# Performance work log

Measured on AMD Instinct MI355X. Metric: run time of the kernel, lower is better.

The kernel has to match this reference:

```python
import jax, jax.numpy as jnp
import numpy as np

N = 100000
E = 1600000
F_IN = 128
H = 128
NUM_GRAPHS = 512
EPS = 1e-5


def setup_inputs() -> dict:
    key = jax.random.key(0)
    ks = jax.random.split(key, 16)
    x = jax.random.normal(ks[0], (N, F_IN), dtype=jnp.float32)
    edge_index = jax.random.randint(ks[1], (2, E), 0, N, dtype=jnp.int32)
    batch = jnp.sort(jax.random.randint(ks[2], (N,), 0, NUM_GRAPHS, dtype=jnp.int32))
    def lin(k, fi, fo):
        s = 1.0 / np.sqrt(fi)
        return jax.random.uniform(k, (fi, fo), jnp.float32, -s, s)
    return {
        "x": x, "edge_index": edge_index, "batch": batch,
        "W1": lin(ks[3], F_IN, H), "b1": jnp.zeros((H,), jnp.float32),
        "g1": jnp.ones((H,), jnp.float32), "beta1": jnp.zeros((H,), jnp.float32),
        "W2": lin(ks[4], H, H), "b2": jnp.zeros((H,), jnp.float32),
        "g2": jnp.ones((H,), jnp.float32), "beta2": jnp.zeros((H,), jnp.float32),
        "W3": lin(ks[5], H, H), "b3": jnp.zeros((H,), jnp.float32),
        "g3": jnp.ones((H,), jnp.float32), "beta3": jnp.zeros((H,), jnp.float32),
        "Wl": lin(ks[6], H, 1), "bl": jnp.zeros((1,), jnp.float32),
    }


def _layer_norm(x, g, b):
    mu = jnp.mean(x, axis=-1, keepdims=True)
    var = jnp.mean((x - mu) ** 2, axis=-1, keepdims=True)
    return (x - mu) * jax.lax.rsqrt(var + EPS) * g + b


def _gcn_conv(x, W, b, src, dst, dinv):
    # GCNConv: D^{-1/2}(A+I)D^{-1/2} X W + b, deg includes self-loops
    h = x @ W                                   # [N,H]
    enorm = dinv[src] * dinv[dst]               # [E]
    agg = jax.ops.segment_sum(h[src] * enorm[:, None], dst, num_segments=N)
    agg = agg + h * (dinv * dinv)[:, None]      # self-loop contribution
    return agg + b


def reference(x, edge_index, batch, W1, b1, g1, beta1, W2, b2, g2, beta2,
              W3, b3, g3, beta3, Wl, bl):
    src, dst = edge_index[0], edge_index[1]
    deg = 1.0 + jax.ops.segment_sum(jnp.ones((E,), jnp.float32), dst, num_segments=N)
    dinv = jax.lax.rsqrt(deg)
    h = jax.nn.relu(_layer_norm(_gcn_conv(x, W1, b1, src, dst, dinv), g1, beta1))
    h = jax.nn.relu(_layer_norm(_gcn_conv(h, W2, b2, src, dst, dinv), g2, beta2))
    h = jax.nn.relu(_layer_norm(_gcn_conv(h, W3, b3, src, dst, dinv), g3, beta3))
    # global mean pool over graphs
    sums = jax.ops.segment_sum(h, batch, num_segments=NUM_GRAPHS)
    cnts = jax.ops.segment_sum(jnp.ones((N,), jnp.float32), batch, num_segments=NUM_GRAPHS)
    pooled = sums / jnp.maximum(cnts, 1.0)[:, None]
    return pooled @ Wl + bl                     # [NUM_GRAPHS, 1]
```

## Files before the change

kernel.cpp:

```cpp
#include <hip/hip_runtime.h>
#include <hip/hip_bf16.h>
#include <math.h>

#define N_NODES    100000
#define N_EDGES    1600000
#define FDIM       128
#define NUM_GRAPHS 512
#define EPS        1e-5f
#define PADN       100096

#define B_CVT   12512
#define B_WPK   192

#define NBUCK   196
#define CAPA    10240
#define EB_CHUNK 8192
#define BINA_BLOCKS ((N_EDGES + EB_CHUNK - 1) / EB_CHUNK)

typedef __attribute__((ext_vector_type(8))) __bf16 bf16x8;
typedef __attribute__((ext_vector_type(4))) float  f32x4;

__device__ __forceinline__ unsigned short f2bf(float f) {
    unsigned u = __builtin_bit_cast(unsigned, f);
    u += 0x7FFF + ((u >> 16) & 1);
    return (unsigned short)(u >> 16);
}
__device__ __forceinline__ float bf2f(unsigned short b) {
    unsigned u = ((unsigned)b) << 16;
    return __builtin_bit_cast(float, u);
}

__device__ __forceinline__ void dec4(unsigned dw, float* o) {
    auto lo = __builtin_amdgcn_cvt_pk_f32_fp8(dw, false);
    auto hi = __builtin_amdgcn_cvt_pk_f32_fp8(dw, true);
    o[0] = lo[0]; o[1] = lo[1]; o[2] = hi[0]; o[3] = hi[1];
}

__device__ __forceinline__ void acc16(uint4 v, float* a) {
    float d[16];
    dec4(v.x, &d[0]); dec4(v.y, &d[4]); dec4(v.z, &d[8]); dec4(v.w, &d[12]);
#pragma unroll
    for (int f = 0; f < 16; f++) a[f] += d[f];
}


__global__ __launch_bounds__(256) void k_build(const int* __restrict__ src,
                                               const int* __restrict__ dst,
                                               int* __restrict__ bcur,
                                               unsigned* __restrict__ binned,
                                               const float* __restrict__ x,
                                               unsigned short* __restrict__ xb,
                                               const float* __restrict__ W1,
                                               const float* __restrict__ W2,
                                               const float* __restrict__ W3,
                                               unsigned short* __restrict__ wp) {
    int b = blockIdx.x;
    int t = threadIdx.x;
    if (b < BINA_BLOCKS) {
        __shared__ int hist[NBUCK];
        __shared__ int lbase[NBUCK];
        __shared__ int loff[NBUCK];
        int e0 = b * EB_CHUNK;

        for (int j = t; j < NBUCK; j += 256) { hist[j] = 0; loff[j] = 0; }
        __syncthreads();

        for (int k = t; k < EB_CHUNK; k += 256) {
            int e = e0 + k;
            if (e < N_EDGES) atomicAdd(&hist[dst[e] >> 9], 1);
        }
        __syncthreads();
        for (int j = t; j < NBUCK; j += 256)
            lbase[j] = atomicAdd(&bcur[j], hist[j]);
        __syncthreads();

        for (int k = t; k < EB_CHUNK; k += 256) {
            int e = e0 + k;
            if (e < N_EDGES) {
                int d = dst[e];
                int bk = d >> 9;
                int p = lbase[bk] + atomicAdd(&loff[bk], 1);
                binned[(size_t)bk * CAPA + p] = (unsigned)src[e] | ((unsigned)(d & 511) << 17);
            }
        }
    } else if (b < BINA_BLOCKS + B_CVT) {
        long long idx = ((long long)(b - BINA_BLOCKS) * 256 + t) * 4;
        ushort4 o;
        if (idx < (long long)N_NODES * FDIM) {
            float4 v = *(const float4*)(x + idx);
            o.x = f2bf(v.x); o.y = f2bf(v.y); o.z = f2bf(v.z); o.w = f2bf(v.w);
        } else {
            o.x = o.y = o.z = o.w = 0;
        }
        *(ushort4*)(xb + idx) = o;
    } else {
        int wb  = b - (BINA_BLOCKS + B_CVT);
        int mat = wb >> 6;
        const float* W = (mat == 0) ? W1 : (mat == 1) ? W2 : W3;
        unsigned short* o = wp + (size_t)mat * 16384;
        int idx = (wb & 63) * 256 + t;
        int j  = idx & 7;
        int l  = (idx >> 3) & 63;
        int ct = (idx >> 9) & 7;
        int ks = idx >> 12;
        int k  = ks * 32 + (l >> 4) * 8 + j;
        int c  = ct * 16 + (l & 15);
        o[idx] = f2bf(W[k * 128 + c]);
    }
}


__global__ __launch_bounds__(256) void k_bscan(const int* __restrict__ bcur,
                                               int* __restrict__ bbase,
                                               int* __restrict__ offs) {
    __shared__ int lds[256];
    int t = threadIdx.x;
    int v = (t < NBUCK) ? bcur[t] : 0;
    lds[t] = v;
    __syncthreads();
    for (int off = 1; off < 256; off <<= 1) {
        int y = 0;
        if (t >= off) y = lds[t - off];
        __syncthreads();
        if (t >= off) lds[t] += y;
        __syncthreads();
    }
    if (t < NBUCK) bbase[t] = lds[t] - v;
    if (t == 0) offs[N_NODES] = N_EDGES;
}


__global__ __launch_bounds__(256) void k_binB(const unsigned* __restrict__ binned,
                                              const int* __restrict__ bcur,
                                              const int* __restrict__ bbase,
                                              int* __restrict__ offs,
                                              float* __restrict__ dinv,
                                              int* __restrict__ csr_src) {
    __shared__ int cnt_l[512];
    __shared__ int lofs[512];
    __shared__ int part[256];
    __shared__ int stage[CAPA];
    int b = blockIdx.x;
    int t = threadIdx.x;
    int nb0 = b * 512;
    int cnt = bcur[b];
    int seg0 = bbase[b];

    cnt_l[t] = 0; cnt_l[t + 256] = 0;
    __syncthreads();

    for (int k = t; k < cnt; k += 256)
        atomicAdd(&cnt_l[binned[(size_t)b * CAPA + k] >> 17], 1);
    __syncthreads();

    int c0 = cnt_l[2 * t], c1 = cnt_l[2 * t + 1];
    int ps = c0 + c1;
    part[t] = ps;
    __syncthreads();
    for (int off = 1; off < 256; off <<= 1) {
        int y = 0;
        if (t >= off) y = part[t - off];
        __syncthreads();
        if (t >= off) part[t] += y;
        __syncthreads();
    }
    int excl = part[t] - ps;
    lofs[2 * t]     = excl;
    lofs[2 * t + 1] = excl + c0;
    __syncthreads();

    for (int j = t; j < 512; j += 256) {
        int node = nb0 + j;
        if (node < N_NODES) {
            offs[node] = seg0 + lofs[j];
            dinv[node] = rsqrtf(1.0f + (float)cnt_l[j]);
        }
    }
    __syncthreads();

    for (int k = t; k < cnt; k += 256) {
        unsigned v = binned[(size_t)b * CAPA + k];
        int ld = v >> 17;
        int p  = atomicAdd(&lofs[ld], 1);
        stage[p] = (int)(v & 0x1FFFF);
    }
    __syncthreads();
    for (int k = t; k < cnt; k += 256) csr_src[seg0 + k] = stage[k];
}


__global__ __launch_bounds__(256) void k_gemm(const unsigned short* __restrict__ A,
                                              const unsigned short* __restrict__ Wp,
                                              const float* __restrict__ dinv,
                                              unsigned char* __restrict__ C8) {
    int t    = threadIdx.x;
    int lane = t & 63;
    int w    = t >> 6;
    int wc   = w & 1;
    int wr   = w >> 1;
    int rb   = blockIdx.x * 128 + wr * 64 + (lane & 15);
    int koff = (lane >> 4) * 8;

    f32x4 acc[4][4];
#pragma unroll
    for (int c = 0; c < 4; c++)
#pragma unroll
        for (int r = 0; r < 4; r++) acc[c][r] = (f32x4){0.f, 0.f, 0.f, 0.f};

    const bf16x8* Wv = (const bf16x8*)Wp;
#pragma unroll
    for (int ks = 0; ks < 4; ++ks) {
        bf16x8 fw[4], fa[4];
#pragma unroll
        for (int c = 0; c < 4; ++c)
            fw[c] = Wv[(ks * 8 + wc * 4 + c) * 64 + lane];
#pragma unroll
        for (int r = 0; r < 4; ++r) {
            const uint4 v = *(const uint4*)(A + (size_t)(rb + r * 16) * 128 + ks * 32 + koff);
            fa[r] = __builtin_bit_cast(bf16x8, v);
        }
#pragma unroll
        for (int c = 0; c < 4; ++c)
#pragma unroll
            for (int r = 0; r < 4; ++r)
                acc[c][r] = __builtin_amdgcn_mfma_f32_16x16x32_bf16(fw[c], fa[r], acc[c][r], 0, 0, 0);
    }

#pragma unroll
    for (int r = 0; r < 4; ++r) {
        int row = blockIdx.x * 128 + wr * 64 + r * 16 + (lane & 15);
        if (row < N_NODES) {
            float dv = dinv[row];
#pragma unroll
            for (int c = 0; c < 4; ++c) {
                int col = (wc * 4 + c) * 16 + (lane >> 4) * 4;
                unsigned u = __builtin_amdgcn_cvt_pk_fp8_f32(acc[c][r][0] * dv, acc[c][r][1] * dv, 0, false);
                u = (unsigned)__builtin_amdgcn_cvt_pk_fp8_f32(acc[c][r][2] * dv, acc[c][r][3] * dv, (int)u, true);
                *(unsigned*)(C8 + (size_t)row * 128 + col) = u;
            }
        }
    }
}


__global__ __launch_bounds__(256) void k_agg(const unsigned char* __restrict__ h8,
                                             unsigned short* __restrict__ out,
                                             const int* __restrict__ offs,
                                             const int* __restrict__ csr_src,
                                             const float* __restrict__ dinv,
                                             const float* __restrict__ bias,
                                             const float* __restrict__ gamma,
                                             const float* __restrict__ beta) {
    int t    = threadIdx.x;
    int lane = t & 63;
    int grp  = lane >> 3;
    int sl   = lane & 7;
    int i    = blockIdx.x * 32 + (t >> 6) * 8 + grp;

    float di = dinv[i];
    size_t lofs16 = (size_t)sl * 16;

    float a[16];
    {
        uint4 v = *(const uint4*)(h8 + (size_t)i * 128 + lofs16);
        float d[16];
        dec4(v.x, &d[0]); dec4(v.y, &d[4]); dec4(v.z, &d[8]); dec4(v.w, &d[12]);
#pragma unroll
        for (int f = 0; f < 16; f++) a[f] = d[f];
    }

    int e0 = offs[i], e1 = offs[i + 1];
    int e = e0;
    for (; e + 4 <= e1; e += 4) {
        int s0 = csr_src[e + 0];
        int s1 = csr_src[e + 1];
        int s2 = csr_src[e + 2];
        int s3 = csr_src[e + 3];
        uint4 v0 = *(const uint4*)(h8 + (size_t)s0 * 128 + lofs16);
        uint4 v1 = *(const uint4*)(h8 + (size_t)s1 * 128 + lofs16);
        uint4 v2 = *(const uint4*)(h8 + (size_t)s2 * 128 + lofs16);
        uint4 v3 = *(const uint4*)(h8 + (size_t)s3 * 128 + lofs16);
        acc16(v0, a); acc16(v1, a); acc16(v2, a); acc16(v3, a);
    }
    for (; e < e1; ++e) {
        int s = csr_src[e];
        uint4 v = *(const uint4*)(h8 + (size_t)s * 128 + lofs16);
        acc16(v, a);
    }

    float4 b0 = *(const float4*)(bias + sl * 16);
    float4 b1 = *(const float4*)(bias + sl * 16 + 4);
    float4 b2 = *(const float4*)(bias + sl * 16 + 8);
    float4 b3 = *(const float4*)(bias + sl * 16 + 12);
    a[0]  = fmaf(a[0],  di, b0.x); a[1]  = fmaf(a[1],  di, b0.y);
    a[2]  = fmaf(a[2],  di, b0.z); a[3]  = fmaf(a[3],  di, b0.w);
    a[4]  = fmaf(a[4],  di, b1.x); a[5]  = fmaf(a[5],  di, b1.y);
    a[6]  = fmaf(a[6],  di, b1.z); a[7]  = fmaf(a[7],  di, b1.w);
    a[8]  = fmaf(a[8],  di, b2.x); a[9]  = fmaf(a[9],  di, b2.y);
    a[10] = fmaf(a[10], di, b2.z); a[11] = fmaf(a[11], di, b2.w);
    a[12] = fmaf(a[12], di, b3.x); a[13] = fmaf(a[13], di, b3.y);
    a[14] = fmaf(a[14], di, b3.z); a[15] = fmaf(a[15], di, b3.w);

    float s1 = 0.f, s2 = 0.f;
#pragma unroll
    for (int f = 0; f < 16; f++) { s1 += a[f]; s2 += a[f] * a[f]; }
#pragma unroll
    for (int off = 1; off < 8; off <<= 1) {
        s1 += __shfl_xor(s1, off);
        s2 += __shfl_xor(s2, off);
    }
    float mu   = s1 * (1.0f / 128.0f);
    float var  = s2 * (1.0f / 128.0f) - mu * mu;
    float rstd = rsqrtf(var + EPS);

    float g[16], be[16];
    {
        float4 g0 = *(const float4*)(gamma + sl * 16);
        float4 g1 = *(const float4*)(gamma + sl * 16 + 4);
        float4 g2 = *(const float4*)(gamma + sl * 16 + 8);
        float4 g3 = *(const float4*)(gamma + sl * 16 + 12);
        g[0]=g0.x; g[1]=g0.y; g[2]=g0.z; g[3]=g0.w;
        g[4]=g1.x; g[5]=g1.y; g[6]=g1.z; g[7]=g1.w;
        g[8]=g2.x; g[9]=g2.y; g[10]=g2.z; g[11]=g2.w;
        g[12]=g3.x; g[13]=g3.y; g[14]=g3.z; g[15]=g3.w;
        float4 e0v = *(const float4*)(beta + sl * 16);
        float4 e1v = *(const float4*)(beta + sl * 16 + 4);
        float4 e2v = *(const float4*)(beta + sl * 16 + 8);
        float4 e3v = *(const float4*)(beta + sl * 16 + 12);
        be[0]=e0v.x; be[1]=e0v.y; be[2]=e0v.z; be[3]=e0v.w;
        be[4]=e1v.x; be[5]=e1v.y; be[6]=e1v.z; be[7]=e1v.w;
        be[8]=e2v.x; be[9]=e2v.y; be[10]=e2v.z; be[11]=e2v.w;
        be[12]=e3v.x; be[13]=e3v.y; be[14]=e3v.z; be[15]=e3v.w;
    }

    unsigned ow[8];
#pragma unroll
    for (int f = 0; f < 8; f++) {
        float r0 = fmaxf((a[2*f]   - mu) * rstd * g[2*f]   + be[2*f],   0.f);
        float r1 = fmaxf((a[2*f+1] - mu) * rstd * g[2*f+1] + be[2*f+1], 0.f);
        ow[f] = (unsigned)f2bf(r0) | ((unsigned)f2bf(r1) << 16);
    }
    uint4* op = (uint4*)(out + (size_t)i * 128 + sl * 16);
    op[0] = make_uint4(ow[0], ow[1], ow[2], ow[3]);
    op[1] = make_uint4(ow[4], ow[5], ow[6], ow[7]);
}


__global__ __launch_bounds__(256) void k_pool(const unsigned short* __restrict__ h,
                                              const int* __restrict__ batch,
                                              const float* __restrict__ Wl,
                                              const float* __restrict__ bl,
                                              float* __restrict__ out) {
    __shared__ float2 part[4][64];
    int g = blockIdx.x;
    int t = threadIdx.x, w = t >> 6, lane = t & 63;

    int lo = 0, hi = N_NODES;
    while (lo < hi) { int mid = (lo + hi) >> 1; if (batch[mid] < g) lo = mid + 1; else hi = mid; }
    int s = lo;
    lo = s; hi = N_NODES;
    while (lo < hi) { int mid = (lo + hi) >> 1; if (batch[mid] < g + 1) lo = mid + 1; else hi = mid; }
    int e = lo;

    float ax = 0.f, ay = 0.f;
    for (int n = s + w; n < e; n += 4) {
        unsigned v = *(const unsigned*)(h + (size_t)n * 128 + lane * 2);
        ax += bf2f((unsigned short)(v & 0xffff));
        ay += bf2f((unsigned short)(v >> 16));
    }
    part[w][lane] = make_float2(ax, ay);
    __syncthreads();
    if (t < 64) {
        float sx = part[0][lane].x + part[1][lane].x + part[2][lane].x + part[3][lane].x;
        float sy = part[0][lane].y + part[1][lane].y + part[2][lane].y + part[3][lane].y;
        float cnt = fmaxf((float)(e - s), 1.0f);
        float inv = 1.0f / cnt;
        float p = sx * inv * Wl[lane * 2] + sy * inv * Wl[lane * 2 + 1];
#pragma unroll
        for (int off = 32; off; off >>= 1) p += __shfl_xor(p, off);
        if (lane == 0) out[g] = p + bl[0];
    }
}


extern "C" void kernel_launch(void* const* d_in, const int* in_sizes, int n_in,
                              void* d_out, int out_size, void* d_ws, size_t ws_size,
                              hipStream_t stream) {
    const float* x     = (const float*)d_in[0];
    const int*   ei    = (const int*)d_in[1];
    const int*   batch = (const int*)d_in[2];
    const float* W1 = (const float*)d_in[3];
    const float* b1 = (const float*)d_in[4];
    const float* g1 = (const float*)d_in[5];
    const float* be1 = (const float*)d_in[6];
    const float* W2 = (const float*)d_in[7];
    const float* b2 = (const float*)d_in[8];
    const float* g2 = (const float*)d_in[9];
    const float* be2 = (const float*)d_in[10];
    const float* W3 = (const float*)d_in[11];
    const float* b3 = (const float*)d_in[12];
    const float* g3 = (const float*)d_in[13];
    const float* be3 = (const float*)d_in[14];
    const float* Wl = (const float*)d_in[15];
    const float* bl = (const float*)d_in[16];

    const int* src = ei;
    const int* dst = ei + N_EDGES;

    char* ws = (char*)d_ws;
    size_t off = 0;
    auto alloc = [&](size_t bytes) -> void* {
        void* p = ws + off;
        off += (bytes + 255) & ~(size_t)255;
        return p;
    };
    unsigned short* xb   = (unsigned short*)alloc((size_t)PADN * FDIM * 2);
    unsigned short* hA   = (unsigned short*)alloc((size_t)PADN * FDIM * 2);
    unsigned char*  hF   = (unsigned char*)alloc((size_t)PADN * FDIM);
    unsigned short* wp   = (unsigned short*)alloc((size_t)3 * 16384 * 2);
    float* dinv    = (float*)alloc((size_t)N_NODES * 4);
    int*   offs    = (int*)alloc((size_t)(N_NODES + 1) * 4);
    int*   csr_src = (int*)alloc((size_t)N_EDGES * 4);
    unsigned* binned = (unsigned*)alloc((size_t)NBUCK * CAPA * 4);
    int*   bcur    = (int*)alloc(256 * 4);
    int*   bbase   = (int*)alloc(256 * 4);

    hipMemsetAsync(bcur, 0, 256 * 4, stream);

    k_build<<<BINA_BLOCKS + B_CVT + B_WPK, 256, 0, stream>>>(src, dst, bcur, binned,
                                                             x, xb, W1, W2, W3, wp);
    k_bscan<<<1, 256, 0, stream>>>(bcur, bbase, offs);
    k_binB<<<NBUCK, 256, 0, stream>>>(binned, bcur, bbase, offs, dinv, csr_src);

    int gemm_grid = PADN / 128;
    int agg_grid  = N_NODES / 32;

    k_gemm<<<gemm_grid, 256, 0, stream>>>(xb, wp, dinv, hF);
    k_agg<<<agg_grid, 256, 0, stream>>>(hF, hA, offs, csr_src, dinv, b1, g1, be1);
    k_gemm<<<gemm_grid, 256, 0, stream>>>(hA, wp + 16384, dinv, hF);
    k_agg<<<agg_grid, 256, 0, stream>>>(hF, hA, offs, csr_src, dinv, b2, g2, be2);
    k_gemm<<<gemm_grid, 256, 0, stream>>>(hA, wp + 32768, dinv, hF);
    k_agg<<<agg_grid, 256, 0, stream>>>(hF, hA, offs, csr_src, dinv, b3, g3, be3);

    k_pool<<<NUM_GRAPHS, 256, 0, stream>>>(hA, batch, Wl, bl, (float*)d_out);
}
```

Measured before the change: 276.0 us.

## Stage edges in LDS during binning, fold bucket scan into binB, unroll aggregation

The edge binning pass now reads src/dst once, keeps the packed values and bucket ids in shared memory, and reuses them for the scatter step. It also uses smaller chunks so more blocks run in parallel. The separate single-block bucket scan kernel is removed, and each binB block instead computes its own segment base with a wave-reduced prefix over bcur. The aggregation gather loop gains an 8-way unrolled stage so more loads are in flight. The trade-off is smaller chunks, which mean more global atomics on bcur and a less contiguous scatter order, plus extra shared memory and registers.

```diff
diff --git a/kernel.cpp b/kernel.cpp
--- a/kernel.cpp
+++ b/kernel.cpp
@@ -14,7 +14,7 @@
 
 #define NBUCK   196
 #define CAPA    10240
-#define EB_CHUNK 8192
+#define EB_CHUNK 2048
 #define BINA_BLOCKS ((N_EDGES + EB_CHUNK - 1) / EB_CHUNK)
 
 typedef __attribute__((ext_vector_type(8))) __bf16 bf16x8;
@@ -60,28 +60,31 @@
         __shared__ int hist[NBUCK];
         __shared__ int lbase[NBUCK];
         __shared__ int loff[NBUCK];
+        __shared__ unsigned lpack[EB_CHUNK];
+        __shared__ unsigned short lbuck[EB_CHUNK];
         int e0 = b * EB_CHUNK;
+        int nE = min(EB_CHUNK, N_EDGES - e0);
 
         for (int j = t; j < NBUCK; j += 256) { hist[j] = 0; loff[j] = 0; }
         __syncthreads();
 
-        for (int k = t; k < EB_CHUNK; k += 256) {
-            int e = e0 + k;
-            if (e < N_EDGES) atomicAdd(&hist[dst[e] >> 9], 1);
+        for (int k = t; k < nE; k += 256) {
+            int e  = e0 + k;
+            int d  = dst[e];
+            int bk = d >> 9;
+            lpack[k] = (unsigned)src[e] | ((unsigned)(d & 511) << 17);
+            lbuck[k] = (unsigned short)bk;
+            atomicAdd(&hist[bk], 1);
         }
         __syncthreads();
         for (int j = t; j < NBUCK; j += 256)
             lbase[j] = atomicAdd(&bcur[j], hist[j]);
         __syncthreads();
 
-        for (int k = t; k < EB_CHUNK; k += 256) {
-            int e = e0 + k;
-            if (e < N_EDGES) {
-                int d = dst[e];
-                int bk = d >> 9;
-                int p = lbase[bk] + atomicAdd(&loff[bk], 1);
-                binned[(size_t)bk * CAPA + p] = (unsigned)src[e] | ((unsigned)(d & 511) << 17);
-            }
+        for (int k = t; k < nE; k += 256) {
+            int bk = lbuck[k];
+            int p  = lbase[bk] + atomicAdd(&loff[bk], 1);
+            binned[(size_t)bk * CAPA + p] = lpack[k];
         }
     } else if (b < BINA_BLOCKS + B_CVT) {
         long long idx = ((long long)(b - BINA_BLOCKS) * 256 + t) * 4;
@@ -110,29 +113,8 @@
 }
 
 
-__global__ __launch_bounds__(256) void k_bscan(const int* __restrict__ bcur,
-                                               int* __restrict__ bbase,
-                                               int* __restrict__ offs) {
-    __shared__ int lds[256];
-    int t = threadIdx.x;
-    int v = (t < NBUCK) ? bcur[t] : 0;
-    lds[t] = v;
-    __syncthreads();
-    for (int off = 1; off < 256; off <<= 1) {
-        int y = 0;
-        if (t >= off) y = lds[t - off];
-        __syncthreads();
-        if (t >= off) lds[t] += y;
-        __syncthreads();
-    }
-    if (t < NBUCK) bbase[t] = lds[t] - v;
-    if (t == 0) offs[N_NODES] = N_EDGES;
-}
-
-
 __global__ __launch_bounds__(256) void k_binB(const unsigned* __restrict__ binned,
                                               const int* __restrict__ bcur,
-                                              const int* __restrict__ bbase,
                                               int* __restrict__ offs,
                                               float* __restrict__ dinv,
                                               int* __restrict__ csr_src) {
@@ -144,7 +126,19 @@
     int t = threadIdx.x;
     int nb0 = b * 512;
     int cnt = bcur[b];
-    int seg0 = bbase[b];
+
+    int pv = (t < b) ? bcur[t] : 0;
+#pragma unroll
+    for (int off = 32; off; off >>= 1) pv += __shfl_down(pv, off);
+    part[t >> 6] = pv;
+    __syncthreads();
+    int seg0 = part[0];
+    if (t == 0) {
+    }
+    __syncthreads();
+    if ((t & 63) == 0) part[t >> 6] = pv;
+    __syncthreads();
+    seg0 = part[0] + part[1] + part[2] + part[3];
 
     cnt_l[t] = 0; cnt_l[t + 256] = 0;
     __syncthreads();
@@ -176,6 +170,7 @@
             dinv[node] = rsqrtf(1.0f + (float)cnt_l[j]);
         }
     }
+    if (b == NBUCK - 1 && t == 0) offs[N_NODES] = N_EDGES;
     __syncthreads();
 
     for (int k = t; k < cnt; k += 256) {
@@ -271,6 +266,26 @@
 
     int e0 = offs[i], e1 = offs[i + 1];
     int e = e0;
+    for (; e + 8 <= e1; e += 8) {
+        int s0 = csr_src[e + 0];
+        int s1 = csr_src[e + 1];
+        int s2 = csr_src[e + 2];
+        int s3 = csr_src[e + 3];
+        int s4 = csr_src[e + 4];
+        int s5 = csr_src[e + 5];
+        int s6 = csr_src[e + 6];
+        int s7 = csr_src[e + 7];
+        uint4 v0 = *(const uint4*)(h8 + (size_t)s0 * 128 + lofs16);
+        uint4 v1 = *(const uint4*)(h8 + (size_t)s1 * 128 + lofs16);
+        uint4 v2 = *(const uint4*)(h8 + (size_t)s2 * 128 + lofs16);
+        uint4 v3 = *(const uint4*)(h8 + (size_t)s3 * 128 + lofs16);
+        uint4 v4 = *(const uint4*)(h8 + (size_t)s4 * 128 + lofs16);
+        uint4 v5 = *(const uint4*)(h8 + (size_t)s5 * 128 + lofs16);
+        uint4 v6 = *(const uint4*)(h8 + (size_t)s6 * 128 + lofs16);
+        uint4 v7 = *(const uint4*)(h8 + (size_t)s7 * 128 + lofs16);
+        acc16(v0, a); acc16(v1, a); acc16(v2, a); acc16(v3, a);
+        acc16(v4, a); acc16(v5, a); acc16(v6, a); acc16(v7, a);
+    }
     for (; e + 4 <= e1; e += 4) {
         int s0 = csr_src[e + 0];
         int s1 = csr_src[e + 1];
@@ -423,14 +438,12 @@
     int*   csr_src = (int*)alloc((size_t)N_EDGES * 4);
     unsigned* binned = (unsigned*)alloc((size_t)NBUCK * CAPA * 4);
     int*   bcur    = (int*)alloc(256 * 4);
-    int*   bbase   = (int*)alloc(256 * 4);
 
     hipMemsetAsync(bcur, 0, 256 * 4, stream);
 
     k_build<<<BINA_BLOCKS + B_CVT + B_WPK, 256, 0, stream>>>(src, dst, bcur, binned,
                                                              x, xb, W1, W2, W3, wp);
-    k_bscan<<<1, 256, 0, stream>>>(bcur, bbase, offs);
-    k_binB<<<NBUCK, 256, 0, stream>>>(binned, bcur, bbase, offs, dinv, csr_src);
+    k_binB<<<NBUCK, 256, 0, stream>>>(binned, bcur, offs, dinv, csr_src);
 
     int gemm_grid = PADN / 128;
     int agg_grid  = N_NODES / 32;
```

After: 280.2 us. No clear change (+1.5%).
